# Kernel optimization log

Hardware: AMD Instinct MI355X
Metric: run time of the kernel (lower is better)

## Reference

```python
import jax, jax.numpy as jnp
import numpy as np

B, S, D = 16, 512, 13 * 768  # batch, pad_size, (num_layers+1)*hidden
H1, H2 = 1000, 40


def setup_inputs() -> dict:
    key = jax.random.key(0)
    k = jax.random.split(key, 5)
    hidden_states = jax.random.normal(k[0], (B, S, D), dtype=jnp.float32)
    # monotonically increasing subword start indices; 0 == padding slot
    token_starts = jnp.sort(jax.random.randint(k[1], (B, S), 0, S), axis=1).astype(jnp.int64)
    W1 = jax.random.normal(k[2], (D, H1), dtype=jnp.float32) * 0.02
    b1 = jnp.zeros((H1,), dtype=jnp.float32)
    W2 = jax.random.normal(k[3], (H1, H2), dtype=jnp.float32) * 0.02
    b2 = jnp.zeros((H2,), dtype=jnp.float32)
    W3 = jax.random.normal(k[4], (H2, 1), dtype=jnp.float32) * 0.02
    b3 = jnp.zeros((1,), dtype=jnp.float32)
    return {"hidden_states": hidden_states, "token_starts": token_starts,
            "W1": W1, "b1": b1, "W2": W2, "b2": b2, "W3": W3, "b3": b3}


def reference(hidden_states, token_starts, W1, b1, W2, b2, W3, b3):
    # MLP head over concatenated per-layer hidden states: [B,S,D] -> [B,S]
    h = jax.nn.relu(jnp.einsum('bsd,dh->bsh', hidden_states, W1) + b1)
    h = jax.nn.relu(jnp.einsum('bsh,hk->bsk', h, W2) + b2)
    pred_logits = jax.nn.sigmoid(jnp.einsum('bsk,ko->bso', h, W3) + b3)[..., 0]  # [B,S]
    # ragged gather: pred_labels[b,w] = pred_logits[b, token_starts[b,w]] if start != 0 else 0
    gathered = jnp.take_along_axis(pred_logits, token_starts, axis=1)
    pred_labels = jnp.where(token_starts != 0, gathered, jnp.float32(0.0))
    return pred_labels
```

## Files before the change

### kernel.cpp

```cpp
#include <hip/hip_runtime.h>

typedef __bf16 bf16x8 __attribute__((ext_vector_type(8)));
typedef float  f32x4  __attribute__((ext_vector_type(4)));

#define D_DIM 9984
#define H1P   1024
#define M_DIM 8192

__device__ __forceinline__ void gld_lds16(const void* g, void* l) {
  __builtin_amdgcn_global_load_lds((__attribute__((address_space(1))) void*)(g),
                                   (__attribute__((address_space(3))) void*)(l),
                                   16, 0, 0);
}

__global__ __launch_bounds__(256) void k_cvt_a(const float* __restrict__ A,
                                               __bf16* __restrict__ Ab) {
  const size_t t = (size_t)blockIdx.x * 256 + threadIdx.x;
  const float4* p = (const float4*)A + t * 2;
  const float4 a = p[0], b = p[1];
  bf16x8 o;
  o[0] = (__bf16)a.x; o[1] = (__bf16)a.y; o[2] = (__bf16)a.z; o[3] = (__bf16)a.w;
  o[4] = (__bf16)b.x; o[5] = (__bf16)b.y; o[6] = (__bf16)b.z; o[7] = (__bf16)b.w;
  *(bf16x8*)(Ab + t * 8) = o;
}

__global__ __launch_bounds__(256) void k_transpose_w1(const float* __restrict__ W1,
                                                      __bf16* __restrict__ W1T) {
  __shared__ float tile[32][33];
  const int bk = blockIdx.x, bn = blockIdx.y;
  const int tx = threadIdx.x, ty = threadIdx.y;
#pragma unroll
  for (int i = 0; i < 4; ++i) {
    const int kk = bk * 32 + ty + i * 8;
    const int nn = bn * 32 + tx;
    tile[ty + i * 8][tx] = (nn < 1000) ? W1[(size_t)kk * 1000 + nn] : 0.f;
  }
  __syncthreads();
#pragma unroll
  for (int i = 0; i < 4; ++i) {
    const int nn = bn * 32 + ty + i * 8;
    const int kk = bk * 32 + tx;
    W1T[(size_t)nn * D_DIM + kk] = (__bf16)tile[tx][ty + i * 8];
  }
}

__global__ void k_prep_w2(const float* __restrict__ W2, __bf16* __restrict__ W2T) {
  const int idx = blockIdx.x * 256 + threadIdx.x;
  const int j = idx >> 10, k = idx & 1023;
  const float v = (j < 40 && k < 1000) ? W2[k * 40 + j] : 0.f;
  W2T[idx] = (__bf16)v;
}

__global__ __launch_bounds__(256) void k_gemm1b(const __bf16* __restrict__ A,
                                                const __bf16* __restrict__ BT,
                                                const float* __restrict__ b1,
                                                __bf16* __restrict__ C) {
  __shared__ __bf16 As[128 * 32];
  __shared__ __bf16 Bs[128 * 32];
  const int tid  = threadIdx.x;
  const int lane = tid & 63;
  const int wid  = tid >> 6;
  const int tm = blockIdx.x, tn = blockIdx.y;
  const int wm = wid & 1, wn = wid >> 1;

  const int c0 = wid * 2, c1 = c0 + 1;
  const int lr = lane >> 2;
  const int lc = (lane & 3) * 8;
  const __bf16* ag0 = A  + (size_t)(tm * 128 + c0 * 16 + lr) * D_DIM + lc;
  const __bf16* ag1 = A  + (size_t)(tm * 128 + c1 * 16 + lr) * D_DIM + lc;
  const __bf16* bg0 = BT + (size_t)(tn * 128 + c0 * 16 + lr) * D_DIM + lc;
  const __bf16* bg1 = BT + (size_t)(tn * 128 + c1 * 16 + lr) * D_DIM + lc;
  __bf16* al0 = &As[c0 * 16 * 32];
  __bf16* al1 = &As[c1 * 16 * 32];
  __bf16* bl0 = &Bs[c0 * 16 * 32];
  __bf16* bl1 = &Bs[c1 * 16 * 32];

  const int fr = lane & 15;
  const int kq = (lane >> 4) * 8;
  f32x4 acc[4][4] = {};

  for (int i = 0; i < 312; ++i) {
    const size_t k0 = (size_t)i * 32;
    __syncthreads();
    gld_lds16(ag0 + k0, al0);
    gld_lds16(ag1 + k0, al1);
    gld_lds16(bg0 + k0, bl0);
    gld_lds16(bg1 + k0, bl1);
    __syncthreads();
    bf16x8 af[4], bf[4];
#pragma unroll
    for (int mi = 0; mi < 4; ++mi)
      af[mi] = *(const bf16x8*)&As[(wm * 64 + mi * 16 + fr) * 32 + kq];
#pragma unroll
    for (int ni = 0; ni < 4; ++ni)
      bf[ni] = *(const bf16x8*)&Bs[(wn * 64 + ni * 16 + fr) * 32 + kq];
#pragma unroll
    for (int mi = 0; mi < 4; ++mi)
#pragma unroll
      for (int ni = 0; ni < 4; ++ni)
        acc[mi][ni] = __builtin_amdgcn_mfma_f32_16x16x32_bf16(af[mi], bf[ni], acc[mi][ni], 0, 0, 0);
  }

  const int row0 = tm * 128 + wm * 64 + ((lane >> 4) << 2);
  const int col0 = tn * 128 + wn * 64 + fr;
#pragma unroll
  for (int ni = 0; ni < 4; ++ni) {
    const int col = col0 + ni * 16;
    const float bias = (col < 1000) ? b1[col] : 0.f;
#pragma unroll
    for (int mi = 0; mi < 4; ++mi)
#pragma unroll
      for (int r = 0; r < 4; ++r) {
        const float v = acc[mi][ni][r] + bias;
        C[(size_t)(row0 + mi * 16 + r) * H1P + col] = (__bf16)fmaxf(v, 0.f);
      }
  }
}

__global__ __launch_bounds__(256) void k_gemm1(const float* __restrict__ A,
                                               const __bf16* __restrict__ BT,
                                               const float* __restrict__ b1,
                                               __bf16* __restrict__ C) {
  __shared__ __bf16 As[128 * 32];
  __shared__ __bf16 Bs[128 * 32];
  const int tid  = threadIdx.x;
  const int lane = tid & 63;
  const int wid  = tid >> 6;
  const int tm = blockIdx.x, tn = blockIdx.y;
  const int wm = wid & 1, wn = wid >> 1;

  const int arow = tid >> 1;
  const int acol = (tid & 1) * 16;
  const float* ag = A + (size_t)(tm * 128 + arow) * D_DIM + acol;
  __bf16* asw = &As[arow * 32 + acol];

  const int c0 = wid * 2, c1 = wid * 2 + 1;
  const __bf16* bg0 = BT + (size_t)(tn * 128 + c0 * 16 + (lane >> 2)) * D_DIM + (lane & 3) * 8;
  const __bf16* bg1 = BT + (size_t)(tn * 128 + c1 * 16 + (lane >> 2)) * D_DIM + (lane & 3) * 8;
  __bf16* bl0 = &Bs[c0 * 16 * 32];
  __bf16* bl1 = &Bs[c1 * 16 * 32];

  const int fr = lane & 15;
  const int kq = (lane >> 4) * 8;
  f32x4 acc[4][4] = {};

  float4 pa[4];
  {
    const float4* ap = (const float4*)ag;
    pa[0] = ap[0]; pa[1] = ap[1]; pa[2] = ap[2]; pa[3] = ap[3];
  }
  for (int i = 0; i < 312; ++i) {
    const int k0 = i * 32;
    __syncthreads();
    {
      const float* pf = (const float*)pa;
      bf16x8 w0, w1;
#pragma unroll
      for (int j = 0; j < 8; ++j) { w0[j] = (__bf16)pf[j]; w1[j] = (__bf16)pf[j + 8]; }
      *(bf16x8*)asw       = w0;
      *(bf16x8*)(asw + 8) = w1;
    }
    gld_lds16(bg0 + k0, bl0);
    gld_lds16(bg1 + k0, bl1);
    __syncthreads();
    if (i != 311) {
      const float4* ap = (const float4*)(ag + k0 + 32);
      pa[0] = ap[0]; pa[1] = ap[1]; pa[2] = ap[2]; pa[3] = ap[3];
    }
    bf16x8 af[4], bf[4];
#pragma unroll
    for (int mi = 0; mi < 4; ++mi)
      af[mi] = *(const bf16x8*)&As[(wm * 64 + mi * 16 + fr) * 32 + kq];
#pragma unroll
    for (int ni = 0; ni < 4; ++ni)
      bf[ni] = *(const bf16x8*)&Bs[(wn * 64 + ni * 16 + fr) * 32 + kq];
#pragma unroll
    for (int mi = 0; mi < 4; ++mi)
#pragma unroll
      for (int ni = 0; ni < 4; ++ni)
        acc[mi][ni] = __builtin_amdgcn_mfma_f32_16x16x32_bf16(af[mi], bf[ni], acc[mi][ni], 0, 0, 0);
  }
  const int row0 = tm * 128 + wm * 64 + ((lane >> 4) << 2);
  const int col0 = tn * 128 + wn * 64 + fr;
#pragma unroll
  for (int ni = 0; ni < 4; ++ni) {
    const int col = col0 + ni * 16;
    const float bias = (col < 1000) ? b1[col] : 0.f;
#pragma unroll
    for (int mi = 0; mi < 4; ++mi)
#pragma unroll
      for (int r = 0; r < 4; ++r) {
        const float v = acc[mi][ni][r] + bias;
        C[(size_t)(row0 + mi * 16 + r) * H1P + col] = (__bf16)fmaxf(v, 0.f);
      }
  }
}

__global__ __launch_bounds__(256) void k_gemm2l(const __bf16* __restrict__ h1,
                                                const __bf16* __restrict__ W2T,
                                                const float* __restrict__ b2,
                                                const float* __restrict__ W3,
                                                const float* __restrict__ b3,
                                                float* __restrict__ lg) {
  __shared__ __bf16 As[64 * 32];
  __shared__ __bf16 Bs[64 * 32];
  const int tid  = threadIdx.x;
  const int lane = tid & 63;
  const int wid  = tid >> 6;
  const int bm   = blockIdx.x;

  const __bf16* ag = h1  + (size_t)(bm * 64 + wid * 16 + (lane >> 2)) * H1P + (lane & 3) * 8;
  const __bf16* bg = W2T + (size_t)(wid * 16 + (lane >> 2)) * H1P + (lane & 3) * 8;
  __bf16* al = &As[wid * 16 * 32];
  __bf16* bl = &Bs[wid * 16 * 32];

  const int fr = lane & 15;
  const int kq = (lane >> 4) * 8;
  f32x4 acc[4] = {};

  for (int i = 0; i < 32; ++i) {
    const int k0 = i * 32;
    __syncthreads();
    gld_lds16(ag + k0, al);
    gld_lds16(bg + k0, bl);
    __syncthreads();
    const bf16x8 a = *(const bf16x8*)&As[(wid * 16 + fr) * 32 + kq];
#pragma unroll
    for (int ni = 0; ni < 4; ++ni) {
      const bf16x8 b = *(const bf16x8*)&Bs[(ni * 16 + fr) * 32 + kq];
      acc[ni] = __builtin_amdgcn_mfma_f32_16x16x32_bf16(a, b, acc[ni], 0, 0, 0);
    }
  }
  float s[4] = {0.f, 0.f, 0.f, 0.f};
#pragma unroll
  for (int ni = 0; ni < 4; ++ni) {
    const int j = ni * 16 + fr;
    if (j < 40) {
      const float w3 = W3[j], bias = b2[j];
#pragma unroll
      for (int r = 0; r < 4; ++r)
        s[r] += fmaxf(acc[ni][r] + bias, 0.f) * w3;
    }
  }
#pragma unroll
  for (int off = 1; off < 16; off <<= 1)
#pragma unroll
    for (int r = 0; r < 4; ++r)
      s[r] += __shfl_xor(s[r], off, 16);
  if (fr == 0) {
    const int m0 = bm * 64 + wid * 16 + ((lane >> 4) << 2);
    const float b3v = b3[0];
#pragma unroll
    for (int r = 0; r < 4; ++r)
      lg[m0 + r] = 1.f / (1.f + __expf(-(s[r] + b3v)));
  }
}

__global__ void k_gather(const int* __restrict__ ts, const float* __restrict__ lg,
                         float* __restrict__ out) {
  const int t = blockIdx.x * 256 + threadIdx.x;
  const int b = t >> 9;
  const int s = ts[t];
  out[t] = (s > 0 && s < 512) ? lg[(b << 9) + s] : 0.f;
}

extern "C" void kernel_launch(void* const* d_in, const int* in_sizes, int n_in,
                              void* d_out, int out_size, void* d_ws, size_t ws_size,
                              hipStream_t stream) {
  const float* hs = (const float*)d_in[0];
  const int*   ts = (const int*)d_in[1];
  const float* W1 = (const float*)d_in[2];
  const float* b1 = (const float*)d_in[3];
  const float* W2 = (const float*)d_in[4];
  const float* b2 = (const float*)d_in[5];
  const float* W3 = (const float*)d_in[6];
  const float* b3 = (const float*)d_in[7];
  float* out = (float*)d_out;
  char* ws = (char*)d_ws;

  const size_t ABF = 163577856;
  const size_t NEED = ABF + 20447232 + 16777216 + 131072 + 32768;

  if (ws_size >= NEED) {
    __bf16* Ab  = (__bf16*)(ws);
    __bf16* W1T = (__bf16*)(ws + ABF);
    __bf16* h1  = (__bf16*)(ws + ABF + 20447232);
    __bf16* W2T = (__bf16*)(ws + ABF + 20447232 + 16777216);
    float*  lg  = (float*) (ws + ABF + 20447232 + 16777216 + 131072);

    k_cvt_a<<<39936, 256, 0, stream>>>(hs, Ab);
    k_transpose_w1<<<dim3(312, 32), dim3(32, 8), 0, stream>>>(W1, W1T);
    k_prep_w2<<<256, 256, 0, stream>>>(W2, W2T);
    k_gemm1b<<<dim3(64, 8), 256, 0, stream>>>(Ab, W1T, b1, h1);
    k_gemm2l<<<128, 256, 0, stream>>>(h1, W2T, b2, W3, b3, lg);
    k_gather<<<32, 256, 0, stream>>>(ts, lg, out);
  } else {
    __bf16* W1T = (__bf16*)(ws);
    __bf16* h1  = (__bf16*)(ws + 20447232);
    __bf16* W2T = (__bf16*)(ws + 20447232 + 16777216);
    float*  lg  = (float*) (ws + 20447232 + 16777216 + 131072);

    k_transpose_w1<<<dim3(312, 32), dim3(32, 8), 0, stream>>>(W1, W1T);
    k_prep_w2<<<256, 256, 0, stream>>>(W2, W2T);
    k_gemm1<<<dim3(64, 8), 256, 0, stream>>>(hs, W1T, b1, h1);
    k_gemm2l<<<128, 256, 0, stream>>>(h1, W2T, b2, W3, b3, lg);
    k_gather<<<32, 256, 0, stream>>>(ts, lg, out);
  }
}
```

Before: 724.6 us.

## Fuse fp32-to-bf16 conversion into double-buffered GEMM1 and drop separate convert pass

Removes the standalone activation conversion kernel and its bf16 workspace copy, so GEMM1 always reads fp32 hidden states and converts them in registers. GEMM1 and GEMM2 switch to double-buffered shared memory with one barrier per K step, which lets the next tile's loads overlap the current tile's MFMA work. GEMM1's grid is swapped so blocks that share the same A rows are launched next to each other, which should improve L2 reuse of the large activation matrix. The cost is twice the LDS per block and A tiles going through registers instead of the direct global-to-LDS load path.

```diff
diff --git a/kernel.cpp b/kernel.cpp
--- a/kernel.cpp
+++ b/kernel.cpp
@@ -5,23 +5,11 @@
 
 #define D_DIM 9984
 #define H1P   1024
-#define M_DIM 8192
 
 __device__ __forceinline__ void gld_lds16(const void* g, void* l) {
   __builtin_amdgcn_global_load_lds((__attribute__((address_space(1))) void*)(g),
                                    (__attribute__((address_space(3))) void*)(l),
                                    16, 0, 0);
-}
-
-__global__ __launch_bounds__(256) void k_cvt_a(const float* __restrict__ A,
-                                               __bf16* __restrict__ Ab) {
-  const size_t t = (size_t)blockIdx.x * 256 + threadIdx.x;
-  const float4* p = (const float4*)A + t * 2;
-  const float4 a = p[0], b = p[1];
-  bf16x8 o;
-  o[0] = (__bf16)a.x; o[1] = (__bf16)a.y; o[2] = (__bf16)a.z; o[3] = (__bf16)a.w;
-  o[4] = (__bf16)b.x; o[5] = (__bf16)b.y; o[6] = (__bf16)b.z; o[7] = (__bf16)b.w;
-  *(bf16x8*)(Ab + t * 8) = o;
 }
 
 __global__ __launch_bounds__(256) void k_transpose_w1(const float* __restrict__ W1,
@@ -51,94 +39,29 @@
   W2T[idx] = (__bf16)v;
 }
 
-__global__ __launch_bounds__(256) void k_gemm1b(const __bf16* __restrict__ A,
+__global__ __launch_bounds__(256) void k_gemm1f(const float* __restrict__ A,
                                                 const __bf16* __restrict__ BT,
                                                 const float* __restrict__ b1,
                                                 __bf16* __restrict__ C) {
-  __shared__ __bf16 As[128 * 32];
-  __shared__ __bf16 Bs[128 * 32];
+  __shared__ __align__(16) __bf16 As[2][128 * 32];
+  __shared__ __align__(16) __bf16 Bs[2][128 * 32];
   const int tid  = threadIdx.x;
   const int lane = tid & 63;
   const int wid  = tid >> 6;
-  const int tm = blockIdx.x, tn = blockIdx.y;
+  const int tn = blockIdx.x, tm = blockIdx.y;
   const int wm = wid & 1, wn = wid >> 1;
+
+  const int arow = tid >> 1;
+  const int acol = (tid & 1) * 16;
+  const float* ag = A + (size_t)(tm * 128 + arow) * D_DIM + acol;
+  const int aoff = arow * 32 + acol;
 
   const int c0 = wid * 2, c1 = c0 + 1;
   const int lr = lane >> 2;
   const int lc = (lane & 3) * 8;
-  const __bf16* ag0 = A  + (size_t)(tm * 128 + c0 * 16 + lr) * D_DIM + lc;
-  const __bf16* ag1 = A  + (size_t)(tm * 128 + c1 * 16 + lr) * D_DIM + lc;
   const __bf16* bg0 = BT + (size_t)(tn * 128 + c0 * 16 + lr) * D_DIM + lc;
   const __bf16* bg1 = BT + (size_t)(tn * 128 + c1 * 16 + lr) * D_DIM + lc;
-  __bf16* al0 = &As[c0 * 16 * 32];
-  __bf16* al1 = &As[c1 * 16 * 32];
-  __bf16* bl0 = &Bs[c0 * 16 * 32];
-  __bf16* bl1 = &Bs[c1 * 16 * 32];
-
-  const int fr = lane & 15;
-  const int kq = (lane >> 4) * 8;
-  f32x4 acc[4][4] = {};
-
-  for (int i = 0; i < 312; ++i) {
-    const size_t k0 = (size_t)i * 32;
-    __syncthreads();
-    gld_lds16(ag0 + k0, al0);
-    gld_lds16(ag1 + k0, al1);
-    gld_lds16(bg0 + k0, bl0);
-    gld_lds16(bg1 + k0, bl1);
-    __syncthreads();
-    bf16x8 af[4], bf[4];
-#pragma unroll
-    for (int mi = 0; mi < 4; ++mi)
-      af[mi] = *(const bf16x8*)&As[(wm * 64 + mi * 16 + fr) * 32 + kq];
-#pragma unroll
-    for (int ni = 0; ni < 4; ++ni)
-      bf[ni] = *(const bf16x8*)&Bs[(wn * 64 + ni * 16 + fr) * 32 + kq];
-#pragma unroll
-    for (int mi = 0; mi < 4; ++mi)
-#pragma unroll
-      for (int ni = 0; ni < 4; ++ni)
-        acc[mi][ni] = __builtin_amdgcn_mfma_f32_16x16x32_bf16(af[mi], bf[ni], acc[mi][ni], 0, 0, 0);
-  }
-
-  const int row0 = tm * 128 + wm * 64 + ((lane >> 4) << 2);
-  const int col0 = tn * 128 + wn * 64 + fr;
-#pragma unroll
-  for (int ni = 0; ni < 4; ++ni) {
-    const int col = col0 + ni * 16;
-    const float bias = (col < 1000) ? b1[col] : 0.f;
-#pragma unroll
-    for (int mi = 0; mi < 4; ++mi)
-#pragma unroll
-      for (int r = 0; r < 4; ++r) {
-        const float v = acc[mi][ni][r] + bias;
-        C[(size_t)(row0 + mi * 16 + r) * H1P + col] = (__bf16)fmaxf(v, 0.f);
-      }
-  }
-}
-
-__global__ __launch_bounds__(256) void k_gemm1(const float* __restrict__ A,
-                                               const __bf16* __restrict__ BT,
-                                               const float* __restrict__ b1,
-                                               __bf16* __restrict__ C) {
-  __shared__ __bf16 As[128 * 32];
-  __shared__ __bf16 Bs[128 * 32];
-  const int tid  = threadIdx.x;
-  const int lane = tid & 63;
-  const int wid  = tid >> 6;
-  const int tm = blockIdx.x, tn = blockIdx.y;
-  const int wm = wid & 1, wn = wid >> 1;
-
-  const int arow = tid >> 1;
-  const int acol = (tid & 1) * 16;
-  const float* ag = A + (size_t)(tm * 128 + arow) * D_DIM + acol;
-  __bf16* asw = &As[arow * 32 + acol];
-
-  const int c0 = wid * 2, c1 = wid * 2 + 1;
-  const __bf16* bg0 = BT + (size_t)(tn * 128 + c0 * 16 + (lane >> 2)) * D_DIM + (lane & 3) * 8;
-  const __bf16* bg1 = BT + (size_t)(tn * 128 + c1 * 16 + (lane >> 2)) * D_DIM + (lane & 3) * 8;
-  __bf16* bl0 = &Bs[c0 * 16 * 32];
-  __bf16* bl1 = &Bs[c1 * 16 * 32];
+  const int bo0 = c0 * 16 * 32, bo1 = c1 * 16 * 32;
 
   const int fr = lane & 15;
   const int kq = (lane >> 4) * 8;
@@ -149,37 +72,50 @@
     const float4* ap = (const float4*)ag;
     pa[0] = ap[0]; pa[1] = ap[1]; pa[2] = ap[2]; pa[3] = ap[3];
   }
+  gld_lds16(bg0, &Bs[0][bo0]);
+  gld_lds16(bg1, &Bs[0][bo1]);
+  {
+    const float* pf = (const float*)pa;
+    bf16x8 w0, w1;
+#pragma unroll
+    for (int j = 0; j < 8; ++j) { w0[j] = (__bf16)pf[j]; w1[j] = (__bf16)pf[j + 8]; }
+    *(bf16x8*)&As[0][aoff]     = w0;
+    *(bf16x8*)&As[0][aoff + 8] = w1;
+  }
+  __syncthreads();
+
   for (int i = 0; i < 312; ++i) {
-    const int k0 = i * 32;
-    __syncthreads();
-    {
+    const int cur = i & 1, nxt = cur ^ 1;
+    if (i < 311) {
+      const size_t k0n = (size_t)(i + 1) * 32;
+      const float4* ap = (const float4*)(ag + k0n);
+      pa[0] = ap[0]; pa[1] = ap[1]; pa[2] = ap[2]; pa[3] = ap[3];
+      gld_lds16(bg0 + k0n, &Bs[nxt][bo0]);
+      gld_lds16(bg1 + k0n, &Bs[nxt][bo1]);
+    }
+    bf16x8 af[4], bfr[4];
+#pragma unroll
+    for (int mi = 0; mi < 4; ++mi)
+      af[mi] = *(const bf16x8*)&As[cur][(wm * 64 + mi * 16 + fr) * 32 + kq];
+#pragma unroll
+    for (int ni = 0; ni < 4; ++ni)
+      bfr[ni] = *(const bf16x8*)&Bs[cur][(wn * 64 + ni * 16 + fr) * 32 + kq];
+#pragma unroll
+    for (int mi = 0; mi < 4; ++mi)
+#pragma unroll
+      for (int ni = 0; ni < 4; ++ni)
+        acc[mi][ni] = __builtin_amdgcn_mfma_f32_16x16x32_bf16(af[mi], bfr[ni], acc[mi][ni], 0, 0, 0);
+    if (i < 311) {
       const float* pf = (const float*)pa;
       bf16x8 w0, w1;
 #pragma unroll
       for (int j = 0; j < 8; ++j) { w0[j] = (__bf16)pf[j]; w1[j] = (__bf16)pf[j + 8]; }
-      *(bf16x8*)asw       = w0;
-      *(bf16x8*)(asw + 8) = w1;
-    }
-    gld_lds16(bg0 + k0, bl0);
-    gld_lds16(bg1 + k0, bl1);
+      *(bf16x8*)&As[nxt][aoff]     = w0;
+      *(bf16x8*)&As[nxt][aoff + 8] = w1;
+    }
     __syncthreads();
-    if (i != 311) {
-      const float4* ap = (const float4*)(ag + k0 + 32);
-      pa[0] = ap[0]; pa[1] = ap[1]; pa[2] = ap[2]; pa[3] = ap[3];
-    }
-    bf16x8 af[4], bf[4];
-#pragma unroll
-    for (int mi = 0; mi < 4; ++mi)
-      af[mi] = *(const bf16x8*)&As[(wm * 64 + mi * 16 + fr) * 32 + kq];
-#pragma unroll
-    for (int ni = 0; ni < 4; ++ni)
-      bf[ni] = *(const bf16x8*)&Bs[(wn * 64 + ni * 16 + fr) * 32 + kq];
-#pragma unroll
-    for (int mi = 0; mi < 4; ++mi)
-#pragma unroll
-      for (int ni = 0; ni < 4; ++ni)
-        acc[mi][ni] = __builtin_amdgcn_mfma_f32_16x16x32_bf16(af[mi], bf[ni], acc[mi][ni], 0, 0, 0);
-  }
+  }
+
   const int row0 = tm * 128 + wm * 64 + ((lane >> 4) << 2);
   const int col0 = tn * 128 + wn * 64 + fr;
 #pragma unroll
@@ -202,8 +138,8 @@
                                                 const float* __restrict__ W3,
                                                 const float* __restrict__ b3,
                                                 float* __restrict__ lg) {
-  __shared__ __bf16 As[64 * 32];
-  __shared__ __bf16 Bs[64 * 32];
+  __shared__ __align__(16) __bf16 As[2][64 * 32];
+  __shared__ __align__(16) __bf16 Bs[2][64 * 32];
   const int tid  = threadIdx.x;
   const int lane = tid & 63;
   const int wid  = tid >> 6;
@@ -211,25 +147,29 @@
 
   const __bf16* ag = h1  + (size_t)(bm * 64 + wid * 16 + (lane >> 2)) * H1P + (lane & 3) * 8;
   const __bf16* bg = W2T + (size_t)(wid * 16 + (lane >> 2)) * H1P + (lane & 3) * 8;
-  __bf16* al = &As[wid * 16 * 32];
-  __bf16* bl = &Bs[wid * 16 * 32];
+  const int wo = wid * 16 * 32;
 
   const int fr = lane & 15;
   const int kq = (lane >> 4) * 8;
   f32x4 acc[4] = {};
 
+  gld_lds16(ag, &As[0][wo]);
+  gld_lds16(bg, &Bs[0][wo]);
+  __syncthreads();
+
   for (int i = 0; i < 32; ++i) {
-    const int k0 = i * 32;
+    const int cur = i & 1;
+    if (i < 31) {
+      gld_lds16(ag + (i + 1) * 32, &As[cur ^ 1][wo]);
+      gld_lds16(bg + (i + 1) * 32, &Bs[cur ^ 1][wo]);
+    }
+    const bf16x8 a = *(const bf16x8*)&As[cur][(wid * 16 + fr) * 32 + kq];
+#pragma unroll
+    for (int ni = 0; ni < 4; ++ni) {
+      const bf16x8 b = *(const bf16x8*)&Bs[cur][(ni * 16 + fr) * 32 + kq];
+      acc[ni] = __builtin_amdgcn_mfma_f32_16x16x32_bf16(a, b, acc[ni], 0, 0, 0);
+    }
     __syncthreads();
-    gld_lds16(ag + k0, al);
-    gld_lds16(bg + k0, bl);
-    __syncthreads();
-    const bf16x8 a = *(const bf16x8*)&As[(wid * 16 + fr) * 32 + kq];
-#pragma unroll
-    for (int ni = 0; ni < 4; ++ni) {
-      const bf16x8 b = *(const bf16x8*)&Bs[(ni * 16 + fr) * 32 + kq];
-      acc[ni] = __builtin_amdgcn_mfma_f32_16x16x32_bf16(a, b, acc[ni], 0, 0, 0);
-    }
   }
   float s[4] = {0.f, 0.f, 0.f, 0.f};
 #pragma unroll
@@ -278,32 +218,14 @@
   float* out = (float*)d_out;
   char* ws = (char*)d_ws;
 
-  const size_t ABF = 163577856;
-  const size_t NEED = ABF + 20447232 + 16777216 + 131072 + 32768;
-
-  if (ws_size >= NEED) {
-    __bf16* Ab  = (__bf16*)(ws);
-    __bf16* W1T = (__bf16*)(ws + ABF);
-    __bf16* h1  = (__bf16*)(ws + ABF + 20447232);
-    __bf16* W2T = (__bf16*)(ws + ABF + 20447232 + 16777216);
-    float*  lg  = (float*) (ws + ABF + 20447232 + 16777216 + 131072);
-
-    k_cvt_a<<<39936, 256, 0, stream>>>(hs, Ab);
-    k_transpose_w1<<<dim3(312, 32), dim3(32, 8), 0, stream>>>(W1, W1T);
-    k_prep_w2<<<256, 256, 0, stream>>>(W2, W2T);
-    k_gemm1b<<<dim3(64, 8), 256, 0, stream>>>(Ab, W1T, b1, h1);
-    k_gemm2l<<<128, 256, 0, stream>>>(h1, W2T, b2, W3, b3, lg);
-    k_gather<<<32, 256, 0, stream>>>(ts, lg, out);
-  } else {
-    __bf16* W1T = (__bf16*)(ws);
-    __bf16* h1  = (__bf16*)(ws + 20447232);
-    __bf16* W2T = (__bf16*)(ws + 20447232 + 16777216);
-    float*  lg  = (float*) (ws + 20447232 + 16777216 + 131072);
-
-    k_transpose_w1<<<dim3(312, 32), dim3(32, 8), 0, stream>>>(W1, W1T);
-    k_prep_w2<<<256, 256, 0, stream>>>(W2, W2T);
-    k_gemm1<<<dim3(64, 8), 256, 0, stream>>>(hs, W1T, b1, h1);
-    k_gemm2l<<<128, 256, 0, stream>>>(h1, W2T, b2, W3, b3, lg);
-    k_gather<<<32, 256, 0, stream>>>(ts, lg, out);
-  }
-}
+  __bf16* W1T = (__bf16*)(ws);
+  __bf16* h1  = (__bf16*)(ws + 20447232);
+  __bf16* W2T = (__bf16*)(ws + 20447232 + 16777216);
+  float*  lg  = (float*) (ws + 20447232 + 16777216 + 131072);
+
+  k_transpose_w1<<<dim3(312, 32), dim3(32, 8), 0, stream>>>(W1, W1T);
+  k_prep_w2<<<256, 256, 0, stream>>>(W2, W2T);
+  k_gemm1f<<<dim3(8, 64), 256, 0, stream>>>(hs, W1T, b1, h1);
+  k_gemm2l<<<128, 256, 0, stream>>>(h1, W2T, b2, W3, b3, lg);
+  k_gather<<<32, 256, 0, stream>>>(ts, lg, out);
+}
```

Result: slower. 937.5 us (+29.4%).

## Split GEMM1 along K into two halves and fuse bias/ReLU reduction into GEMM2

Applied to the files above, without the earlier changes.

GEMM1 is split into two K-halves, doubling the grid so more blocks fill the CUs. Each half writes fp32 partials that the second GEMM sums, adds bias to and applies ReLU to while loading its A tile. The prep kernels are merged into one launch, and the non-split GEMM2 gets LDS double buffering. The cost is extra memory traffic for writing and reading the fp32 partial buffers.

```diff
diff --git a/kernel.cpp b/kernel.cpp
--- a/kernel.cpp
+++ b/kernel.cpp
@@ -5,7 +5,7 @@
 
 #define D_DIM 9984
 #define H1P   1024
-#define M_DIM 8192
+#define KHALF 4992
 
 __device__ __forceinline__ void gld_lds16(const void* g, void* l) {
   __builtin_amdgcn_global_load_lds((__attribute__((address_space(1))) void*)(g),
@@ -13,42 +13,193 @@
                                    16, 0, 0);
 }
 
-__global__ __launch_bounds__(256) void k_cvt_a(const float* __restrict__ A,
-                                               __bf16* __restrict__ Ab) {
-  const size_t t = (size_t)blockIdx.x * 256 + threadIdx.x;
-  const float4* p = (const float4*)A + t * 2;
-  const float4 a = p[0], b = p[1];
-  bf16x8 o;
-  o[0] = (__bf16)a.x; o[1] = (__bf16)a.y; o[2] = (__bf16)a.z; o[3] = (__bf16)a.w;
-  o[4] = (__bf16)b.x; o[5] = (__bf16)b.y; o[6] = (__bf16)b.z; o[7] = (__bf16)b.w;
-  *(bf16x8*)(Ab + t * 8) = o;
-}
-
-__global__ __launch_bounds__(256) void k_transpose_w1(const float* __restrict__ W1,
-                                                      __bf16* __restrict__ W1T) {
+__global__ __launch_bounds__(256) void k_prep(const float* __restrict__ A,
+                                              __bf16* __restrict__ Ab,
+                                              const float* __restrict__ W1,
+                                              __bf16* __restrict__ W1T,
+                                              const float* __restrict__ W2,
+                                              __bf16* __restrict__ W2T,
+                                              const float* __restrict__ b1,
+                                              float* __restrict__ b1p,
+                                              int abase_blocks) {
   __shared__ float tile[32][33];
-  const int bk = blockIdx.x, bn = blockIdx.y;
-  const int tx = threadIdx.x, ty = threadIdx.y;
-#pragma unroll
-  for (int i = 0; i < 4; ++i) {
-    const int kk = bk * 32 + ty + i * 8;
-    const int nn = bn * 32 + tx;
-    tile[ty + i * 8][tx] = (nn < 1000) ? W1[(size_t)kk * 1000 + nn] : 0.f;
-  }
-  __syncthreads();
-#pragma unroll
-  for (int i = 0; i < 4; ++i) {
-    const int nn = bn * 32 + ty + i * 8;
-    const int kk = bk * 32 + tx;
-    W1T[(size_t)nn * D_DIM + kk] = (__bf16)tile[tx][ty + i * 8];
-  }
-}
-
-__global__ void k_prep_w2(const float* __restrict__ W2, __bf16* __restrict__ W2T) {
-  const int idx = blockIdx.x * 256 + threadIdx.x;
-  const int j = idx >> 10, k = idx & 1023;
-  const float v = (j < 40 && k < 1000) ? W2[k * 40 + j] : 0.f;
-  W2T[idx] = (__bf16)v;
+  const int bx  = blockIdx.x;
+  const int tid = threadIdx.x;
+  if (bx < abase_blocks) {
+    const size_t t = (size_t)bx * 256 + tid;
+    const float4* p = (const float4*)A + t * 2;
+    const float4 a = p[0], b = p[1];
+    bf16x8 o;
+    o[0] = (__bf16)a.x; o[1] = (__bf16)a.y; o[2] = (__bf16)a.z; o[3] = (__bf16)a.w;
+    o[4] = (__bf16)b.x; o[5] = (__bf16)b.y; o[6] = (__bf16)b.z; o[7] = (__bf16)b.w;
+    *(bf16x8*)(Ab + t * 8) = o;
+  } else if (bx < abase_blocks + 9984) {
+    const int b = bx - abase_blocks;
+    const int bk = b % 312, bn = b / 312;
+    const int tx = tid & 31, ty = tid >> 5;
+#pragma unroll
+    for (int i = 0; i < 4; ++i) {
+      const int kk = bk * 32 + ty + i * 8;
+      const int nn = bn * 32 + tx;
+      tile[ty + i * 8][tx] = (nn < 1000) ? W1[(size_t)kk * 1000 + nn] : 0.f;
+    }
+    __syncthreads();
+#pragma unroll
+    for (int i = 0; i < 4; ++i) {
+      const int nn = bn * 32 + ty + i * 8;
+      const int kk = bk * 32 + tx;
+      W1T[(size_t)nn * D_DIM + kk] = (__bf16)tile[tx][ty + i * 8];
+    }
+  } else if (bx < abase_blocks + 9984 + 256) {
+    const int idx = (bx - abase_blocks - 9984) * 256 + tid;
+    const int j = idx >> 10, k = idx & 1023;
+    const float v = (j < 40 && k < 1000) ? W2[k * 40 + j] : 0.f;
+    W2T[idx] = (__bf16)v;
+  } else {
+    for (int i = tid; i < 1024; i += 256)
+      b1p[i] = (i < 1000) ? b1[i] : 0.f;
+  }
+}
+
+__global__ __launch_bounds__(256) void k_gemm1s(const __bf16* __restrict__ A,
+                                                const __bf16* __restrict__ BT,
+                                                float* __restrict__ P) {
+  __shared__ __bf16 As[128 * 32];
+  __shared__ __bf16 Bs[128 * 32];
+  const int tid  = threadIdx.x;
+  const int lane = tid & 63;
+  const int wid  = tid >> 6;
+  const int tm = blockIdx.x, tn = blockIdx.y, kh = blockIdx.z;
+  const int wm = wid & 1, wn = wid >> 1;
+  const size_t kbase = (size_t)kh * KHALF;
+
+  const int c0 = wid * 2, c1 = c0 + 1;
+  const int lr = lane >> 2;
+  const int lc = (lane & 3) * 8;
+  const __bf16* ag0 = A  + (size_t)(tm * 128 + c0 * 16 + lr) * D_DIM + kbase + lc;
+  const __bf16* ag1 = A  + (size_t)(tm * 128 + c1 * 16 + lr) * D_DIM + kbase + lc;
+  const __bf16* bg0 = BT + (size_t)(tn * 128 + c0 * 16 + lr) * D_DIM + kbase + lc;
+  const __bf16* bg1 = BT + (size_t)(tn * 128 + c1 * 16 + lr) * D_DIM + kbase + lc;
+  __bf16* al0 = &As[c0 * 16 * 32];
+  __bf16* al1 = &As[c1 * 16 * 32];
+  __bf16* bl0 = &Bs[c0 * 16 * 32];
+  __bf16* bl1 = &Bs[c1 * 16 * 32];
+
+  const int fr = lane & 15;
+  const int kq = (lane >> 4) * 8;
+  f32x4 acc[4][4] = {};
+
+  for (int i = 0; i < 156; ++i) {
+    const size_t k0 = (size_t)i * 32;
+    __syncthreads();
+    gld_lds16(ag0 + k0, al0);
+    gld_lds16(ag1 + k0, al1);
+    gld_lds16(bg0 + k0, bl0);
+    gld_lds16(bg1 + k0, bl1);
+    __syncthreads();
+    bf16x8 af[4], bfr[4];
+#pragma unroll
+    for (int mi = 0; mi < 4; ++mi)
+      af[mi] = *(const bf16x8*)&As[(wm * 64 + mi * 16 + fr) * 32 + kq];
+#pragma unroll
+    for (int ni = 0; ni < 4; ++ni)
+      bfr[ni] = *(const bf16x8*)&Bs[(wn * 64 + ni * 16 + fr) * 32 + kq];
+#pragma unroll
+    for (int mi = 0; mi < 4; ++mi)
+#pragma unroll
+      for (int ni = 0; ni < 4; ++ni)
+        acc[mi][ni] = __builtin_amdgcn_mfma_f32_16x16x32_bf16(af[mi], bfr[ni], acc[mi][ni], 0, 0, 0);
+  }
+
+  float* Pz = P + (size_t)kh * (8192 * H1P);
+  const int row0 = tm * 128 + wm * 64 + ((lane >> 4) << 2);
+  const int col0 = tn * 128 + wn * 64 + fr;
+#pragma unroll
+  for (int ni = 0; ni < 4; ++ni) {
+    const int col = col0 + ni * 16;
+#pragma unroll
+    for (int mi = 0; mi < 4; ++mi)
+#pragma unroll
+      for (int r = 0; r < 4; ++r)
+        Pz[(size_t)(row0 + mi * 16 + r) * H1P + col] = acc[mi][ni][r];
+  }
+}
+
+__global__ __launch_bounds__(256) void k_gemm2lf(const float* __restrict__ p0,
+                                                 const float* __restrict__ p1,
+                                                 const __bf16* __restrict__ W2T,
+                                                 const float* __restrict__ b1p,
+                                                 const float* __restrict__ b2,
+                                                 const float* __restrict__ W3,
+                                                 const float* __restrict__ b3,
+                                                 float* __restrict__ lg) {
+  __shared__ __align__(16) __bf16 As[64 * 32];
+  __shared__ __align__(16) __bf16 Bs[64 * 32];
+  const int tid  = threadIdx.x;
+  const int lane = tid & 63;
+  const int wid  = tid >> 6;
+  const int bm   = blockIdx.x;
+
+  const size_t abase = (size_t)(bm * 64 + wid * 16 + (lane >> 2)) * H1P + (lane & 3) * 8;
+  const __bf16* bg = W2T + (size_t)(wid * 16 + (lane >> 2)) * H1P + (lane & 3) * 8;
+  const int aoff = (wid * 16 + (lane >> 2)) * 32 + (lane & 3) * 8;
+  __bf16* bl = &Bs[wid * 16 * 32];
+
+  const int fr = lane & 15;
+  const int kq = (lane >> 4) * 8;
+  f32x4 acc[4] = {};
+
+  for (int i = 0; i < 32; ++i) {
+    const int k0 = i * 32;
+    const float4 x0 = *(const float4*)(p0 + abase + k0);
+    const float4 x1 = *(const float4*)(p0 + abase + k0 + 4);
+    const float4 y0 = *(const float4*)(p1 + abase + k0);
+    const float4 y1 = *(const float4*)(p1 + abase + k0 + 4);
+    const float4 c0v = *(const float4*)(b1p + k0 + (lane & 3) * 8);
+    const float4 c1v = *(const float4*)(b1p + k0 + (lane & 3) * 8 + 4);
+    bf16x8 h;
+    h[0] = (__bf16)fmaxf(x0.x + y0.x + c0v.x, 0.f);
+    h[1] = (__bf16)fmaxf(x0.y + y0.y + c0v.y, 0.f);
+    h[2] = (__bf16)fmaxf(x0.z + y0.z + c0v.z, 0.f);
+    h[3] = (__bf16)fmaxf(x0.w + y0.w + c0v.w, 0.f);
+    h[4] = (__bf16)fmaxf(x1.x + y1.x + c1v.x, 0.f);
+    h[5] = (__bf16)fmaxf(x1.y + y1.y + c1v.y, 0.f);
+    h[6] = (__bf16)fmaxf(x1.z + y1.z + c1v.z, 0.f);
+    h[7] = (__bf16)fmaxf(x1.w + y1.w + c1v.w, 0.f);
+    __syncthreads();
+    *(bf16x8*)&As[aoff] = h;
+    gld_lds16(bg + k0, bl);
+    __syncthreads();
+    const bf16x8 a = *(const bf16x8*)&As[(wid * 16 + fr) * 32 + kq];
+#pragma unroll
+    for (int ni = 0; ni < 4; ++ni) {
+      const bf16x8 b = *(const bf16x8*)&Bs[(ni * 16 + fr) * 32 + kq];
+      acc[ni] = __builtin_amdgcn_mfma_f32_16x16x32_bf16(a, b, acc[ni], 0, 0, 0);
+    }
+  }
+  float s[4] = {0.f, 0.f, 0.f, 0.f};
+#pragma unroll
+  for (int ni = 0; ni < 4; ++ni) {
+    const int j = ni * 16 + fr;
+    if (j < 40) {
+      const float w3 = W3[j], bias = b2[j];
+#pragma unroll
+      for (int r = 0; r < 4; ++r)
+        s[r] += fmaxf(acc[ni][r] + bias, 0.f) * w3;
+    }
+  }
+#pragma unroll
+  for (int off = 1; off < 16; off <<= 1)
+#pragma unroll
+    for (int r = 0; r < 4; ++r)
+      s[r] += __shfl_xor(s[r], off, 16);
+  if (fr == 0) {
+    const int m0 = bm * 64 + wid * 16 + ((lane >> 4) << 2);
+    const float b3v = b3[0];
+#pragma unroll
+    for (int r = 0; r < 4; ++r)
+      lg[m0 + r] = 1.f / (1.f + __expf(-(s[r] + b3v)));
+  }
 }
 
 __global__ __launch_bounds__(256) void k_gemm1b(const __bf16* __restrict__ A,
@@ -87,18 +238,18 @@
     gld_lds16(bg0 + k0, bl0);
     gld_lds16(bg1 + k0, bl1);
     __syncthreads();
-    bf16x8 af[4], bf[4];
+    bf16x8 af[4], bfr[4];
 #pragma unroll
     for (int mi = 0; mi < 4; ++mi)
       af[mi] = *(const bf16x8*)&As[(wm * 64 + mi * 16 + fr) * 32 + kq];
 #pragma unroll
     for (int ni = 0; ni < 4; ++ni)
-      bf[ni] = *(const bf16x8*)&Bs[(wn * 64 + ni * 16 + fr) * 32 + kq];
+      bfr[ni] = *(const bf16x8*)&Bs[(wn * 64 + ni * 16 + fr) * 32 + kq];
 #pragma unroll
     for (int mi = 0; mi < 4; ++mi)
 #pragma unroll
       for (int ni = 0; ni < 4; ++ni)
-        acc[mi][ni] = __builtin_amdgcn_mfma_f32_16x16x32_bf16(af[mi], bf[ni], acc[mi][ni], 0, 0, 0);
+        acc[mi][ni] = __builtin_amdgcn_mfma_f32_16x16x32_bf16(af[mi], bfr[ni], acc[mi][ni], 0, 0, 0);
   }
 
   const int row0 = tm * 128 + wm * 64 + ((lane >> 4) << 2);
@@ -114,6 +265,70 @@
         const float v = acc[mi][ni][r] + bias;
         C[(size_t)(row0 + mi * 16 + r) * H1P + col] = (__bf16)fmaxf(v, 0.f);
       }
+  }
+}
+
+__global__ __launch_bounds__(256) void k_gemm2l(const __bf16* __restrict__ h1,
+                                                const __bf16* __restrict__ W2T,
+                                                const float* __restrict__ b2,
+                                                const float* __restrict__ W3,
+                                                const float* __restrict__ b3,
+                                                float* __restrict__ lg) {
+  __shared__ __align__(16) __bf16 As[2][64 * 32];
+  __shared__ __align__(16) __bf16 Bs[2][64 * 32];
+  const int tid  = threadIdx.x;
+  const int lane = tid & 63;
+  const int wid  = tid >> 6;
+  const int bm   = blockIdx.x;
+
+  const __bf16* ag = h1  + (size_t)(bm * 64 + wid * 16 + (lane >> 2)) * H1P + (lane & 3) * 8;
+  const __bf16* bg = W2T + (size_t)(wid * 16 + (lane >> 2)) * H1P + (lane & 3) * 8;
+  const int wo = wid * 16 * 32;
+
+  const int fr = lane & 15;
+  const int kq = (lane >> 4) * 8;
+  f32x4 acc[4] = {};
+
+  gld_lds16(ag, &As[0][wo]);
+  gld_lds16(bg, &Bs[0][wo]);
+  __syncthreads();
+
+  for (int i = 0; i < 32; ++i) {
+    const int cur = i & 1;
+    if (i < 31) {
+      gld_lds16(ag + (i + 1) * 32, &As[cur ^ 1][wo]);
+      gld_lds16(bg + (i + 1) * 32, &Bs[cur ^ 1][wo]);
+    }
+    const bf16x8 a = *(const bf16x8*)&As[cur][(wid * 16 + fr) * 32 + kq];
+#pragma unroll
+    for (int ni = 0; ni < 4; ++ni) {
+      const bf16x8 b = *(const bf16x8*)&Bs[cur][(ni * 16 + fr) * 32 + kq];
+      acc[ni] = __builtin_amdgcn_mfma_f32_16x16x32_bf16(a, b, acc[ni], 0, 0, 0);
+    }
+    __syncthreads();
+  }
+  float s[4] = {0.f, 0.f, 0.f, 0.f};
+#pragma unroll
+  for (int ni = 0; ni < 4; ++ni) {
+    const int j = ni * 16 + fr;
+    if (j < 40) {
+      const float w3 = W3[j], bias = b2[j];
+#pragma unroll
+      for (int r = 0; r < 4; ++r)
+        s[r] += fmaxf(acc[ni][r] + bias, 0.f) * w3;
+    }
+  }
+#pragma unroll
+  for (int off = 1; off < 16; off <<= 1)
+#pragma unroll
+    for (int r = 0; r < 4; ++r)
+      s[r] += __shfl_xor(s[r], off, 16);
+  if (fr == 0) {
+    const int m0 = bm * 64 + wid * 16 + ((lane >> 4) << 2);
+    const float b3v = b3[0];
+#pragma unroll
+    for (int r = 0; r < 4; ++r)
+      lg[m0 + r] = 1.f / (1.f + __expf(-(s[r] + b3v)));
   }
 }
 
@@ -167,18 +382,18 @@
       const float4* ap = (const float4*)(ag + k0 + 32);
       pa[0] = ap[0]; pa[1] = ap[1]; pa[2] = ap[2]; pa[3] = ap[3];
     }
-    bf16x8 af[4], bf[4];
+    bf16x8 af[4], bfr[4];
 #pragma unroll
     for (int mi = 0; mi < 4; ++mi)
       af[mi] = *(const bf16x8*)&As[(wm * 64 + mi * 16 + fr) * 32 + kq];
 #pragma unroll
     for (int ni = 0; ni < 4; ++ni)
-      bf[ni] = *(const bf16x8*)&Bs[(wn * 64 + ni * 16 + fr) * 32 + kq];
+      bfr[ni] = *(const bf16x8*)&Bs[(wn * 64 + ni * 16 + fr) * 32 + kq];
 #pragma unroll
     for (int mi = 0; mi < 4; ++mi)
 #pragma unroll
       for (int ni = 0; ni < 4; ++ni)
-        acc[mi][ni] = __builtin_amdgcn_mfma_f32_16x16x32_bf16(af[mi], bf[ni], acc[mi][ni], 0, 0, 0);
+        acc[mi][ni] = __builtin_amdgcn_mfma_f32_16x16x32_bf16(af[mi], bfr[ni], acc[mi][ni], 0, 0, 0);
   }
   const int row0 = tm * 128 + wm * 64 + ((lane >> 4) << 2);
   const int col0 = tn * 128 + wn * 64 + fr;
@@ -193,66 +408,6 @@
         const float v = acc[mi][ni][r] + bias;
         C[(size_t)(row0 + mi * 16 + r) * H1P + col] = (__bf16)fmaxf(v, 0.f);
       }
-  }
-}
-
-__global__ __launch_bounds__(256) void k_gemm2l(const __bf16* __restrict__ h1,
-                                                const __bf16* __restrict__ W2T,
-                                                const float* __restrict__ b2,
-                                                const float* __restrict__ W3,
-                                                const float* __restrict__ b3,
-                                                float* __restrict__ lg) {
-  __shared__ __bf16 As[64 * 32];
-  __shared__ __bf16 Bs[64 * 32];
-  const int tid  = threadIdx.x;
-  const int lane = tid & 63;
-  const int wid  = tid >> 6;
-  const int bm   = blockIdx.x;
-
-  const __bf16* ag = h1  + (size_t)(bm * 64 + wid * 16 + (lane >> 2)) * H1P + (lane & 3) * 8;
-  const __bf16* bg = W2T + (size_t)(wid * 16 + (lane >> 2)) * H1P + (lane & 3) * 8;
-  __bf16* al = &As[wid * 16 * 32];
-  __bf16* bl = &Bs[wid * 16 * 32];
-
-  const int fr = lane & 15;
-  const int kq = (lane >> 4) * 8;
-  f32x4 acc[4] = {};
-
-  for (int i = 0; i < 32; ++i) {
-    const int k0 = i * 32;
-    __syncthreads();
-    gld_lds16(ag + k0, al);
-    gld_lds16(bg + k0, bl);
-    __syncthreads();
-    const bf16x8 a = *(const bf16x8*)&As[(wid * 16 + fr) * 32 + kq];
-#pragma unroll
-    for (int ni = 0; ni < 4; ++ni) {
-      const bf16x8 b = *(const bf16x8*)&Bs[(ni * 16 + fr) * 32 + kq];
-      acc[ni] = __builtin_amdgcn_mfma_f32_16x16x32_bf16(a, b, acc[ni], 0, 0, 0);
-    }
-  }
-  float s[4] = {0.f, 0.f, 0.f, 0.f};
-#pragma unroll
-  for (int ni = 0; ni < 4; ++ni) {
-    const int j = ni * 16 + fr;
-    if (j < 40) {
-      const float w3 = W3[j], bias = b2[j];
-#pragma unroll
-      for (int r = 0; r < 4; ++r)
-        s[r] += fmaxf(acc[ni][r] + bias, 0.f) * w3;
-    }
-  }
-#pragma unroll
-  for (int off = 1; off < 16; off <<= 1)
-#pragma unroll
-    for (int r = 0; r < 4; ++r)
-      s[r] += __shfl_xor(s[r], off, 16);
-  if (fr == 0) {
-    const int m0 = bm * 64 + wid * 16 + ((lane >> 4) << 2);
-    const float b3v = b3[0];
-#pragma unroll
-    for (int r = 0; r < 4; ++r)
-      lg[m0 + r] = 1.f / (1.f + __expf(-(s[r] + b3v)));
   }
 }
 
@@ -278,30 +433,44 @@
   float* out = (float*)d_out;
   char* ws = (char*)d_ws;
 
-  const size_t ABF = 163577856;
-  const size_t NEED = ABF + 20447232 + 16777216 + 131072 + 32768;
-
-  if (ws_size >= NEED) {
+  const size_t ABF   = 163577856;
+  const size_t W1TSZ = 20447232;
+  const size_t PSZ   = 33554432;
+  const size_t NEED2 = ABF + W1TSZ + 2 * PSZ + 131072 + 4096 + 32768;
+  const size_t NEED1 = ABF + W1TSZ + 16777216 + 131072 + 32768;
+
+  if (ws_size >= NEED2) {
     __bf16* Ab  = (__bf16*)(ws);
     __bf16* W1T = (__bf16*)(ws + ABF);
-    __bf16* h1  = (__bf16*)(ws + ABF + 20447232);
-    __bf16* W2T = (__bf16*)(ws + ABF + 20447232 + 16777216);
-    float*  lg  = (float*) (ws + ABF + 20447232 + 16777216 + 131072);
-
-    k_cvt_a<<<39936, 256, 0, stream>>>(hs, Ab);
-    k_transpose_w1<<<dim3(312, 32), dim3(32, 8), 0, stream>>>(W1, W1T);
-    k_prep_w2<<<256, 256, 0, stream>>>(W2, W2T);
+    float*  p0  = (float*) (ws + ABF + W1TSZ);
+    float*  p1  = (float*) (ws + ABF + W1TSZ + PSZ);
+    __bf16* W2T = (__bf16*)(ws + ABF + W1TSZ + 2 * PSZ);
+    float*  b1p = (float*) (ws + ABF + W1TSZ + 2 * PSZ + 131072);
+    float*  lg  = (float*) (ws + ABF + W1TSZ + 2 * PSZ + 131072 + 4096);
+
+    k_prep<<<39936 + 9984 + 256 + 1, 256, 0, stream>>>(hs, Ab, W1, W1T, W2, W2T, b1, b1p, 39936);
+    k_gemm1s<<<dim3(64, 8, 2), 256, 0, stream>>>(Ab, W1T, p0);
+    k_gemm2lf<<<128, 256, 0, stream>>>(p0, p1, W2T, b1p, b2, W3, b3, lg);
+    k_gather<<<32, 256, 0, stream>>>(ts, lg, out);
+  } else if (ws_size >= NEED1) {
+    __bf16* Ab  = (__bf16*)(ws);
+    __bf16* W1T = (__bf16*)(ws + ABF);
+    __bf16* h1  = (__bf16*)(ws + ABF + W1TSZ);
+    __bf16* W2T = (__bf16*)(ws + ABF + W1TSZ + 16777216);
+    float*  lg  = (float*) (ws + ABF + W1TSZ + 16777216 + 131072);
+
+    k_prep<<<39936 + 9984 + 256, 256, 0, stream>>>(hs, Ab, W1, W1T, W2, W2T, b1, lg, 39936);
     k_gemm1b<<<dim3(64, 8), 256, 0, stream>>>(Ab, W1T, b1, h1);
     k_gemm2l<<<128, 256, 0, stream>>>(h1, W2T, b2, W3, b3, lg);
     k_gather<<<32, 256, 0, stream>>>(ts, lg, out);
   } else {
     __bf16* W1T = (__bf16*)(ws);
-    __bf16* h1  = (__bf16*)(ws + 20447232);
-    __bf16* W2T = (__bf16*)(ws + 20447232 + 16777216);
-    float*  lg  = (float*) (ws + 20447232 + 16777216 + 131072);
-
-    k_transpose_w1<<<dim3(312, 32), dim3(32, 8), 0, stream>>>(W1, W1T);
-    k_prep_w2<<<256, 256, 0, stream>>>(W2, W2T);
+    __bf16* h1  = (__bf16*)(ws + W1TSZ);
+    __bf16* W2T = (__bf16*)(ws + W1TSZ + 16777216);
+    float*  lg  = (float*) (ws + W1TSZ + 16777216 + 131072);
+
+    k_prep<<<9984 + 256, 256, 0, stream>>>(hs, (__bf16*)W1T ,
+                                           W1, W1T, W2, W2T, b1, lg, 0);
     k_gemm1<<<dim3(64, 8), 256, 0, stream>>>(hs, W1T, b1, h1);
     k_gemm2l<<<128, 256, 0, stream>>>(h1, W2T, b2, W3, b3, lg);
     k_gather<<<32, 256, 0, stream>>>(ts, lg, out);
```

New measurement: 760.3 us. 4.9% more time.
